# Performance work log

Measured on AMD Instinct MI355X. Metric: run time of the kernel, lower is better.

The kernel has to match this reference:

```python
import math
import jax, jax.numpy as jnp
import numpy as np

B, N, C = 2, 21760, 256
L, Hh, P = 4, 8, 4
Dh = C // Hh


def setup_inputs() -> dict:
    key = jax.random.key(0)
    ks = jax.random.split(key, 8)
    shapes = np.array([[128, 128], [64, 64], [32, 32], [16, 16]], dtype=np.int64)
    areas = shapes[:, 0] * shapes[:, 1]
    start_ids = np.concatenate([[0], np.cumsum(areas)[:-1]]).astype(np.int64)
    S = int(areas.sum())  # 21760

    in_feats = jax.random.normal(ks[0], (B, N, C), jnp.float32)
    sample_priors = jax.random.uniform(ks[1], (B, N, L, 2), jnp.float32)
    sample_feats = jax.random.normal(ks[2], (B, S, C), jnp.float32)

    # sampling_offsets: zero-init weight in torch; use small random so offsets vary,
    # bias is the canonical deformable-DETR grid init.
    W_off = jax.random.normal(ks[3], (C, Hh * L * P * 2), jnp.float32) * 0.01
    thetas = jnp.arange(Hh, dtype=jnp.float32) * (2.0 * math.pi / Hh)
    grid = jnp.stack([jnp.cos(thetas), jnp.sin(thetas)], axis=1)  # [Hh,2]
    grid = grid / jnp.max(jnp.abs(grid), axis=1, keepdims=True)
    grid = jnp.tile(grid[:, None, None, :], (1, L, P, 1))  # [Hh,L,P,2]
    sizes = jnp.arange(1, P + 1, dtype=jnp.float32).reshape(1, 1, P, 1)
    b_off = (sizes * grid).reshape(-1)  # [Hh*L*P*2]

    W_attn = jax.random.normal(ks[4], (C, Hh * L * P), jnp.float32) * 0.01
    b_attn = jnp.zeros((Hh * L * P,), jnp.float32)
    W_val = jax.random.normal(ks[5], (C, C), jnp.float32) / math.sqrt(C)
    b_val = jnp.zeros((C,), jnp.float32)
    W_out = jax.random.normal(ks[6], (C, C), jnp.float32) / math.sqrt(C)
    b_out = jnp.zeros((C,), jnp.float32)

    return dict(in_feats=in_feats, sample_priors=sample_priors, sample_feats=sample_feats,
                sample_map_shapes=jnp.asarray(shapes), sample_map_start_ids=jnp.asarray(start_ids),
                W_off=W_off, b_off=b_off, W_attn=W_attn, b_attn=b_attn,
                W_val=W_val, b_val=b_val, W_out=W_out, b_out=b_out)


def _msda_core(value, shapes_np, starts_np, loc, attn_w):
    """value: [B,S,Hh,Dh]; loc: [B,N,Hh,L,P,2] in [0,1]; attn_w: [B,N,Hh,L,P].
    Bilinear sampling matching grid_sample(align_corners=False, padding='zeros')."""
    b, n = loc.shape[:2]
    acc = jnp.zeros((b, n, Hh, Dh), value.dtype)
    for l in range(L):
        H_l, W_l = int(shapes_np[l, 0]), int(shapes_np[l, 1])
        s0 = int(starts_np[l])
        v = value[:, s0:s0 + H_l * W_l]  # [B,S_l,Hh,Dh]
        lx = loc[:, :, :, l, :, 0] * W_l - 0.5  # [B,N,Hh,P] pixel coords
        ly = loc[:, :, :, l, :, 1] * H_l - 0.5
        x0f, y0f = jnp.floor(lx), jnp.floor(ly)
        wx1, wy1 = lx - x0f, ly - y0f
        wx0, wy0 = 1.0 - wx1, 1.0 - wy1
        x0, y0 = x0f.astype(jnp.int32), y0f.astype(jnp.int32)

        def gather(xi, yi):
            valid = ((xi >= 0) & (xi < W_l) & (yi >= 0) & (yi < H_l)).astype(v.dtype)
            idx = jnp.clip(yi, 0, H_l - 1) * W_l + jnp.clip(xi, 0, W_l - 1)  # [B,N,Hh,P]
            idx_t = idx.transpose(0, 1, 3, 2).reshape(b, n * P, Hh)
            g = jnp.take_along_axis(v, idx_t[..., None], axis=1)  # [B,N*P,Hh,Dh]
            g = g.reshape(b, n, P, Hh, Dh).transpose(0, 1, 3, 2, 4)  # [B,N,Hh,P,Dh]
            return g * valid[..., None]

        samp = (gather(x0, y0) * (wx0 * wy0)[..., None]
                + gather(x0 + 1, y0) * (wx1 * wy0)[..., None]
                + gather(x0, y0 + 1) * (wx0 * wy1)[..., None]
                + gather(x0 + 1, y0 + 1) * (wx1 * wy1)[..., None])
        acc = acc + jnp.einsum('bnhpd,bnhp->bnhd', samp, attn_w[:, :, :, l, :])
    return acc


def reference(in_feats, sample_priors, sample_feats, sample_map_shapes, sample_map_start_ids,
              W_off, b_off, W_attn, b_attn, W_val, b_val, W_out, b_out):
    b, n = in_feats.shape[:2]
    # structural constants (level geometry)
    shapes_np = np.asarray(jax.device_get(sample_map_shapes))
    starts_np = np.asarray(jax.device_get(sample_map_start_ids))

    off = (in_feats @ W_off + b_off).reshape(b, n, Hh, L, P, 2)
    normalizer = jnp.flip(sample_map_shapes, axis=-1).astype(in_feats.dtype)  # [L,2] (W,H)
    loc = sample_priors[:, :, None, :, None, :] + off / normalizer[None, None, None, :, None, :]

    aw = jax.nn.softmax((in_feats @ W_attn + b_attn).reshape(b, n, Hh, L * P), axis=-1)
    aw = aw.reshape(b, n, Hh, L, P)

    value = (sample_feats @ W_val + b_val).reshape(b, -1, Hh, Dh)
    weighted = _msda_core(value, shapes_np, starts_np, loc, aw)  # [B,N,Hh,Dh]
    out = weighted.reshape(b, n, Hh * Dh) @ W_out + b_out
    return out
```

## Files before the change

kernel.cpp:

```cpp
#include <hip/hip_runtime.h>
#include <cstdint>

constexpr int kB = 2;
constexpr int kN = 21760;
constexpr int kC = 256;
constexpr int kH = 8;
constexpr int kS = 21760;
constexpr int kM = kB * kN;

typedef __attribute__((ext_vector_type(8))) short bf16x8;
typedef __attribute__((ext_vector_type(4))) float f32x4;
typedef __attribute__((ext_vector_type(8))) unsigned short us8;

__device__ __forceinline__ float bf2f(unsigned short u) {
  return __uint_as_float(((unsigned int)u) << 16);
}
__device__ __forceinline__ unsigned short f2bf(float f) {
  unsigned int u = __float_as_uint(f);
  u += 0x7fffu + ((u >> 16) & 1u);
  return (unsigned short)(u >> 16);
}
__device__ __forceinline__ void gld_lds16(const unsigned short* g, unsigned short* l) {
  __builtin_amdgcn_global_load_lds(
      (const __attribute__((address_space(1))) unsigned int*)g,
      (__attribute__((address_space(3))) unsigned int*)l, 16, 0, 0);
}

__global__ __launch_bounds__(256) void convert_act(
    const float* __restrict__ a, const float* __restrict__ b,
    unsigned short* __restrict__ da, unsigned short* __restrict__ db)
{
  const int tid = blockIdx.x * 256 + threadIdx.x;
  const int half = kM * 32;
  const float* src; unsigned short* dst; int id;
  if (tid < half) { src = a; dst = da; id = tid; }
  else            { src = b; dst = db; id = tid - half; }
  const int m = id >> 5;
  const int kb = (id & 31) * 8;
  const float4 x0 = *(const float4*)&src[(size_t)m * 256 + kb];
  const float4 x1 = *(const float4*)&src[(size_t)m * 256 + kb + 4];
  us8 o;
  o[0] = f2bf(x0.x); o[1] = f2bf(x0.y); o[2] = f2bf(x0.z); o[3] = f2bf(x0.w);
  o[4] = f2bf(x1.x); o[5] = f2bf(x1.y); o[6] = f2bf(x1.z); o[7] = f2bf(x1.w);
  *(us8*)&dst[(size_t)m * 256 + (kb ^ ((m & 7) << 3))] = o;
}

__global__ __launch_bounds__(256) void prep_weights(
    const float* __restrict__ Woff, const float* __restrict__ Wattn,
    const float* __restrict__ Wval, const float* __restrict__ Wout,
    unsigned short* __restrict__ BtOff, unsigned short* __restrict__ BtAttn,
    unsigned short* __restrict__ BtVal, unsigned short* __restrict__ BtOut)
{
  const int tid = blockIdx.x * 256 + threadIdx.x;
  const int r = tid >> 5;
  const int kb = (tid & 31) * 8;
  const float* W; unsigned short* Bt; int n, Nn;
  if (r < 256)      { W = Woff;  Bt = BtOff;  n = r;       Nn = 256; }
  else if (r < 384) { W = Wattn; Bt = BtAttn; n = r - 256; Nn = 128; }
  else if (r < 640) { W = Wval;  Bt = BtVal;  n = r - 384; Nn = 256; }
  else              { W = Wout;  Bt = BtOut;  n = r - 640; Nn = 256; }
  us8 o;
#pragma unroll
  for (int i = 0; i < 8; ++i) o[i] = f2bf(W[(size_t)(kb + i) * Nn + n]);
  *(us8*)&Bt[(size_t)n * 256 + (kb ^ ((n & 7) << 3))] = o;
}

template <int OMODE>
__global__ __launch_bounds__(256) void gemm_bf16(
    const unsigned short* __restrict__ A,
    const unsigned short* __restrict__ Bt,
    const float* __restrict__ bias,
    void* __restrict__ Cout, int Nn)
{
  __shared__ unsigned short As[128 * 64];
  __shared__ unsigned short Bs[128 * 64];
  const int t = threadIdx.x;
  const int w = t >> 6, l = t & 63;
  const int m0 = blockIdx.x * 128, n0 = blockIdx.y * 128;
  const int wm = w >> 1, wn = w & 1;

  f32x4 acc[4][4] = {};

  const int srow = l >> 3;
  const int skb  = (l & 7) * 8;

  for (int kt = 0; kt < 256; kt += 64) {
#pragma unroll
    for (int i = 0; i < 4; ++i) {
      const int c = i * 4 + w;
      const int row = c * 8 + srow;
      gld_lds16(A + (size_t)(m0 + row) * 256 + kt + skb, &As[c * 512]);
    }
#pragma unroll
    for (int i = 0; i < 4; ++i) {
      const int c = i * 4 + w;
      const int row = c * 8 + srow;
      gld_lds16(Bt + (size_t)(n0 + row) * 256 + kt + skb, &Bs[c * 512]);
    }
    __syncthreads();

#pragma unroll
    for (int s = 0; s < 2; ++s) {
      bf16x8 af[4], bfr[4];
      const int kf = s * 32 + ((l >> 4) * 8);
#pragma unroll
      for (int i = 0; i < 4; ++i) {
        const int row = wm * 64 + i * 16 + (l & 15);
        af[i] = *(const bf16x8*)&As[row * 64 + (kf ^ ((row & 7) << 3))];
      }
#pragma unroll
      for (int j = 0; j < 4; ++j) {
        const int col = wn * 64 + j * 16 + (l & 15);
        bfr[j] = *(const bf16x8*)&Bs[col * 64 + (kf ^ ((col & 7) << 3))];
      }
#pragma unroll
      for (int i = 0; i < 4; ++i)
#pragma unroll
        for (int j = 0; j < 4; ++j)
          acc[i][j] = __builtin_amdgcn_mfma_f32_16x16x32_bf16(af[i], bfr[j], acc[i][j], 0, 0, 0);
    }
    __syncthreads();
  }

  const int lr = l >> 4;
#pragma unroll
  for (int j = 0; j < 4; ++j) {
    const int col = n0 + wn * 64 + j * 16 + (l & 15);
    const float bv = bias[col];
#pragma unroll
    for (int i = 0; i < 4; ++i) {
      const int rbase = m0 + wm * 64 + i * 16 + lr * 4;
#pragma unroll
      for (int r = 0; r < 4; ++r) {
        const float v = acc[i][j][r] + bv;
        if (OMODE == 0) {
          ((float*)Cout)[(size_t)(rbase + r) * Nn + col] = v;
        } else if (OMODE == 1) {
          ((unsigned short*)Cout)[(size_t)(rbase + r) * Nn + col] = f2bf(v);
        } else {
          const int row = rbase + r;
          const int bb = row >= kS;
          const int s2 = row - bb * kS;
          ((unsigned short*)Cout)[((size_t)(bb * 8 + (col >> 5)) * kS + s2) * 32 + (col & 31)] = f2bf(v);
        }
      }
    }
  }
}

__global__ __launch_bounds__(256) void msda_kernel(
    const unsigned short* __restrict__ off_bf,
    const unsigned short* __restrict__ attn_bf,
    const unsigned short* __restrict__ val_bf,
    const float* __restrict__ priors,
    unsigned short* __restrict__ wgt)
{
  __shared__ int   s_mi[256 * 4];
  __shared__ float s_mw[256 * 4];
  const int q0 = blockIdx.x * 2;
  const int t = threadIdx.x;
  const int qh = t >> 4;
  const int q = q0 + (qh >> 3);
  const int h = qh & 7;

  {
    const int j = t & 15;
    const int lv = j >> 2;

    const float lgt = bf2f(attn_bf[(size_t)q * 128 + h * 16 + j]);
    float mx = lgt;
#pragma unroll
    for (int m = 8; m; m >>= 1) mx = fmaxf(mx, __shfl_xor(mx, m, 16));
    const float p = __expf(lgt - mx);
    float sum = p;
#pragma unroll
    for (int m = 8; m; m >>= 1) sum += __shfl_xor(sum, m, 16);
    const float wN = p / sum;

    const unsigned int oo = *(const unsigned int*)&off_bf[(size_t)q * 256 + (h * 16 + j) * 2];
    const float ox = bf2f((unsigned short)(oo & 0xffff));
    const float oy = bf2f((unsigned short)(oo >> 16));
    const float2 pr = *(const float2*)&priors[(size_t)q * 8 + lv * 2];

    const int Wl = 128 >> lv;
    const float fW = (float)Wl;
    const float lx = fmaf(pr.x, fW, ox) - 0.5f;
    const float ly = fmaf(pr.y, fW, oy) - 0.5f;
    const float x0f = floorf(lx), y0f = floorf(ly);
    const float wx1 = lx - x0f, wy1 = ly - y0f;
    const float wx0 = 1.f - wx1, wy0 = 1.f - wy1;
    const int x0 = (int)x0f, y0 = (int)y0f;
    const int start = (int)((0x5400500040000000ull >> (16 * lv)) & 0xffff);

    const bool vx0 = (x0 >= 0) & (x0 < Wl);
    const bool vx1 = (x0 + 1 >= 0) & (x0 + 1 < Wl);
    const bool vy0 = (y0 >= 0) & (y0 < Wl);
    const bool vy1 = (y0 + 1 >= 0) & (y0 + 1 < Wl);
    const int xc0 = min(max(x0, 0), Wl - 1);
    const int xc1 = min(max(x0 + 1, 0), Wl - 1);
    const int yc0 = min(max(y0, 0), Wl - 1);
    const int yc1 = min(max(y0 + 1, 0), Wl - 1);

    const int off_top = (start + yc0 * Wl + xc0) * 64;
    const int off_bot = (start + yc1 * Wl + xc0) * 64;
    const int dx = (xc1 - xc0) * 64;

    const int slot = j * 16 + (qh ^ (j & 3));
    int4 mi; mi.x = off_top; mi.y = off_bot; mi.z = dx; mi.w = 0;
    *(int4*)&s_mi[slot * 4] = mi;
    float4 mw;
    mw.x = (vx0 & vy0) ? wN * wx0 * wy0 : 0.f;
    mw.y = (vx0 & vy1) ? wN * wx0 * wy1 : 0.f;
    mw.z = (vx1 & vy0) ? wN * wx1 * wy0 : 0.f;
    mw.w = (vx1 & vy1) ? wN * wx1 * wy1 : 0.f;
    *(float4*)&s_mw[slot * 4] = mw;
  }
  __syncthreads();

  const int idx = t & 15;
  const int xsel = idx >> 3;
  const int ch8 = idx & 7;
  const int b = (q >= kN) ? 1 : 0;
  const char* base = (const char*)val_bf + ((size_t)(b * 8 + h) * kS) * 64 + ch8 * 8;

  float a0 = 0.f, a1 = 0.f, a2 = 0.f, a3 = 0.f;
#pragma unroll
  for (int j = 0; j < 16; ++j) {
    const int slot = j * 16 + (qh ^ (j & 3));
    const int4 md = *(const int4*)&s_mi[slot * 4];
    const float2 wv = *(const float2*)&s_mw[slot * 4 + xsel * 2];
    const int dxs = xsel ? md.z : 0;
    const uint2 vt = *(const uint2*)(base + (md.x + dxs));
    const uint2 vb = *(const uint2*)(base + (md.y + dxs));
    a0 = fmaf(wv.x, __uint_as_float(vt.x << 16), a0);
    a1 = fmaf(wv.x, __uint_as_float(vt.x & 0xffff0000u), a1);
    a2 = fmaf(wv.x, __uint_as_float(vt.y << 16), a2);
    a3 = fmaf(wv.x, __uint_as_float(vt.y & 0xffff0000u), a3);
    a0 = fmaf(wv.y, __uint_as_float(vb.x << 16), a0);
    a1 = fmaf(wv.y, __uint_as_float(vb.x & 0xffff0000u), a1);
    a2 = fmaf(wv.y, __uint_as_float(vb.y << 16), a2);
    a3 = fmaf(wv.y, __uint_as_float(vb.y & 0xffff0000u), a3);
  }

  a0 += __shfl_xor(a0, 8, 16);
  a1 += __shfl_xor(a1, 8, 16);
  a2 += __shfl_xor(a2, 8, 16);
  a3 += __shfl_xor(a3, 8, 16);

  if (xsel == 0) {
    const int c0 = h * 32 + ch8 * 4;
    const int dst = (c0 ^ ((q & 7) << 3));
    uint2 o;
    o.x = (unsigned int)f2bf(a0) | ((unsigned int)f2bf(a1) << 16);
    o.y = (unsigned int)f2bf(a2) | ((unsigned int)f2bf(a3) << 16);
    *(uint2*)&wgt[(size_t)q * 256 + dst] = o;
  }
}

extern "C" void kernel_launch(void* const* d_in, const int* in_sizes, int n_in,
                              void* d_out, int out_size, void* d_ws, size_t ws_size,
                              hipStream_t stream) {
  const float* in_feats = (const float*)d_in[0];
  const float* priors   = (const float*)d_in[1];
  const float* sfeats   = (const float*)d_in[2];
  const float* W_off  = (const float*)d_in[5];
  const float* b_off  = (const float*)d_in[6];
  const float* W_attn = (const float*)d_in[7];
  const float* b_attn = (const float*)d_in[8];
  const float* W_val  = (const float*)d_in[9];
  const float* b_val  = (const float*)d_in[10];
  const float* W_out  = (const float*)d_in[11];
  const float* b_out  = (const float*)d_in[12];
  float* out = (float*)d_out;

  unsigned short* in_bf   = (unsigned short*)d_ws;
  unsigned short* s_bf    = in_bf   + (size_t)kM * 256;
  unsigned short* off_bf  = s_bf    + (size_t)kM * 256;
  unsigned short* attn_bf = off_bf  + (size_t)kM * 256;
  unsigned short* val_bf  = attn_bf + (size_t)kM * 128;
  unsigned short* wgt_bf  = val_bf  + (size_t)kM * 256;
  unsigned short* BtOff   = wgt_bf  + (size_t)kM * 256;
  unsigned short* BtAttn  = BtOff   + 256 * 256;
  unsigned short* BtVal   = BtAttn  + 128 * 256;
  unsigned short* BtOut   = BtVal   + 256 * 256;

  const dim3 blk(256);

  convert_act<<<dim3(kM * 32 * 2 / 256), blk, 0, stream>>>(in_feats, sfeats, in_bf, s_bf);
  prep_weights<<<dim3(896 * 32 / 256), blk, 0, stream>>>(
      W_off, W_attn, W_val, W_out, BtOff, BtAttn, BtVal, BtOut);

  gemm_bf16<1><<<dim3(kM / 128, 2), blk, 0, stream>>>(in_bf, BtOff, b_off, off_bf, 256);
  gemm_bf16<1><<<dim3(kM / 128, 1), blk, 0, stream>>>(in_bf, BtAttn, b_attn, attn_bf, 128);
  gemm_bf16<2><<<dim3(kM / 128, 2), blk, 0, stream>>>(s_bf, BtVal, b_val, val_bf, 256);

  msda_kernel<<<dim3(kM / 2), blk, 0, stream>>>(off_bf, attn_bf, val_bf, priors, wgt_bf);

  gemm_bf16<0><<<dim3(kM / 128, 2), blk, 0, stream>>>(wgt_bf, BtOut, b_out, out, 256);
}
```

Baseline: 180.1 us.

## Store offsets/attn head-major and remap MSDA blocks to one head plane per block

The offset and attention GEMMs now write head-major layouts, so each head's 16 logits and 32 offsets sit contiguously per query. The MSDA kernel gives each block 16 queries of a single (batch, head) plane, so the value gathers of neighbouring blocks hit the same plane for better cache locality. Each lane now gathers one corner with 16-byte loads across 8 channels, instead of two 8-byte loads, and partial sums are reduced with two xor-shuffles. The corner records are packed (offset, weight) pairs in padded shared memory. The risk is more shuffle work and the strided head-major writes in the GEMM epilogues.

```diff
diff --git a/kernel.cpp b/kernel.cpp
--- a/kernel.cpp
+++ b/kernel.cpp
@@ -20,6 +20,8 @@
   u += 0x7fffu + ((u >> 16) & 1u);
   return (unsigned short)(u >> 16);
 }
+__device__ __forceinline__ float blo(unsigned int v) { return __uint_as_float(v << 16); }
+__device__ __forceinline__ float bhi(unsigned int v) { return __uint_as_float(v & 0xffff0000u); }
 __device__ __forceinline__ void gld_lds16(const unsigned short* g, unsigned short* l) {
   __builtin_amdgcn_global_load_lds(
       (const __attribute__((address_space(1))) unsigned int*)g,
@@ -133,15 +135,19 @@
 #pragma unroll
       for (int r = 0; r < 4; ++r) {
         const float v = acc[i][j][r] + bv;
+        const int row = rbase + r;
         if (OMODE == 0) {
-          ((float*)Cout)[(size_t)(rbase + r) * Nn + col] = v;
+          ((float*)Cout)[(size_t)row * Nn + col] = v;
         } else if (OMODE == 1) {
-          ((unsigned short*)Cout)[(size_t)(rbase + r) * Nn + col] = f2bf(v);
-        } else {
-          const int row = rbase + r;
+          ((unsigned short*)Cout)[(size_t)row * Nn + col] = f2bf(v);
+        } else if (OMODE == 2) {
           const int bb = row >= kS;
           const int s2 = row - bb * kS;
           ((unsigned short*)Cout)[((size_t)(bb * 8 + (col >> 5)) * kS + s2) * 32 + (col & 31)] = f2bf(v);
+        } else if (OMODE == 3) {
+          ((unsigned short*)Cout)[((size_t)(col >> 4) * kM + row) * 16 + (col & 15)] = f2bf(v);
+        } else {
+          ((unsigned short*)Cout)[((size_t)(col >> 5) * kM + row) * 32 + (col & 31)] = f2bf(v);
         }
       }
     }
@@ -149,25 +155,26 @@
 }
 
 __global__ __launch_bounds__(256) void msda_kernel(
-    const unsigned short* __restrict__ off_bf,
-    const unsigned short* __restrict__ attn_bf,
+    const unsigned short* __restrict__ off_hm,
+    const unsigned short* __restrict__ attn_hm,
     const unsigned short* __restrict__ val_bf,
     const float* __restrict__ priors,
     unsigned short* __restrict__ wgt)
 {
-  __shared__ int   s_mi[256 * 4];
-  __shared__ float s_mw[256 * 4];
-  const int q0 = blockIdx.x * 2;
+  __shared__ int s_rec[16 * 136];
+  const int bid = blockIdx.x;
+  const int plane = bid & 15;
+  const int chunk = bid >> 4;
+  const int b = plane >> 3, h = plane & 7;
   const int t = threadIdx.x;
-  const int qh = t >> 4;
-  const int q = q0 + (qh >> 3);
-  const int h = qh & 7;
+  const int ql = t >> 4;
+  const int q = b * kN + chunk * 16 + ql;
 
   {
     const int j = t & 15;
     const int lv = j >> 2;
 
-    const float lgt = bf2f(attn_bf[(size_t)q * 128 + h * 16 + j]);
+    const float lgt = bf2f(attn_hm[((size_t)h * kM + q) * 16 + j]);
     float mx = lgt;
 #pragma unroll
     for (int m = 8; m; m >>= 1) mx = fmaxf(mx, __shfl_xor(mx, m, 16));
@@ -177,9 +184,9 @@
     for (int m = 8; m; m >>= 1) sum += __shfl_xor(sum, m, 16);
     const float wN = p / sum;
 
-    const unsigned int oo = *(const unsigned int*)&off_bf[(size_t)q * 256 + (h * 16 + j) * 2];
-    const float ox = bf2f((unsigned short)(oo & 0xffff));
-    const float oy = bf2f((unsigned short)(oo >> 16));
+    const unsigned int oo = *(const unsigned int*)&off_hm[((size_t)h * kM + q) * 32 + j * 2];
+    const float ox = blo(oo);
+    const float oy = bhi(oo);
     const float2 pr = *(const float2*)&priors[(size_t)q * 8 + lv * 2];
 
     const int Wl = 128 >> lv;
@@ -201,59 +208,57 @@
     const int yc0 = min(max(y0, 0), Wl - 1);
     const int yc1 = min(max(y0 + 1, 0), Wl - 1);
 
-    const int off_top = (start + yc0 * Wl + xc0) * 64;
-    const int off_bot = (start + yc1 * Wl + xc0) * 64;
-    const int dx = (xc1 - xc0) * 64;
-
-    const int slot = j * 16 + (qh ^ (j & 3));
-    int4 mi; mi.x = off_top; mi.y = off_bot; mi.z = dx; mi.w = 0;
-    *(int4*)&s_mi[slot * 4] = mi;
-    float4 mw;
-    mw.x = (vx0 & vy0) ? wN * wx0 * wy0 : 0.f;
-    mw.y = (vx0 & vy1) ? wN * wx0 * wy1 : 0.f;
-    mw.z = (vx1 & vy0) ? wN * wx1 * wy0 : 0.f;
-    mw.w = (vx1 & vy1) ? wN * wx1 * wy1 : 0.f;
-    *(float4*)&s_mw[slot * 4] = mw;
+    const int rt = start + yc0 * Wl;
+    const int rb = start + yc1 * Wl;
+
+    int4 r0, r1;
+    r0.x = (rt + xc0) * 64; r0.y = __float_as_int((vx0 & vy0) ? wN * wx0 * wy0 : 0.f);
+    r0.z = (rt + xc1) * 64; r0.w = __float_as_int((vx1 & vy0) ? wN * wx1 * wy0 : 0.f);
+    r1.x = (rb + xc0) * 64; r1.y = __float_as_int((vx0 & vy1) ? wN * wx0 * wy1 : 0.f);
+    r1.z = (rb + xc1) * 64; r1.w = __float_as_int((vx1 & vy1) ? wN * wx1 * wy1 : 0.f);
+
+    const int base = ql * 136 + j * 8;
+    *(int4*)&s_rec[base] = r0;
+    *(int4*)&s_rec[base + 4] = r1;
   }
   __syncthreads();
 
-  const int idx = t & 15;
-  const int xsel = idx >> 3;
-  const int ch8 = idx & 7;
-  const int b = (q >= kN) ? 1 : 0;
-  const char* base = (const char*)val_bf + ((size_t)(b * 8 + h) * kS) * 64 + ch8 * 8;
+  const int lane = t & 15;
+  const int c = lane >> 2;
+  const int k = lane & 3;
+  const char* plane_base = (const char*)val_bf + (size_t)plane * kS * 64 + k * 16;
+  const int* rp = &s_rec[ql * 136 + c * 2];
 
   float a0 = 0.f, a1 = 0.f, a2 = 0.f, a3 = 0.f;
+  float a4 = 0.f, a5 = 0.f, a6 = 0.f, a7 = 0.f;
 #pragma unroll
   for (int j = 0; j < 16; ++j) {
-    const int slot = j * 16 + (qh ^ (j & 3));
-    const int4 md = *(const int4*)&s_mi[slot * 4];
-    const float2 wv = *(const float2*)&s_mw[slot * 4 + xsel * 2];
-    const int dxs = xsel ? md.z : 0;
-    const uint2 vt = *(const uint2*)(base + (md.x + dxs));
-    const uint2 vb = *(const uint2*)(base + (md.y + dxs));
-    a0 = fmaf(wv.x, __uint_as_float(vt.x << 16), a0);
-    a1 = fmaf(wv.x, __uint_as_float(vt.x & 0xffff0000u), a1);
-    a2 = fmaf(wv.x, __uint_as_float(vt.y << 16), a2);
-    a3 = fmaf(wv.x, __uint_as_float(vt.y & 0xffff0000u), a3);
-    a0 = fmaf(wv.y, __uint_as_float(vb.x << 16), a0);
-    a1 = fmaf(wv.y, __uint_as_float(vb.x & 0xffff0000u), a1);
-    a2 = fmaf(wv.y, __uint_as_float(vb.y << 16), a2);
-    a3 = fmaf(wv.y, __uint_as_float(vb.y & 0xffff0000u), a3);
-  }
-
-  a0 += __shfl_xor(a0, 8, 16);
-  a1 += __shfl_xor(a1, 8, 16);
-  a2 += __shfl_xor(a2, 8, 16);
-  a3 += __shfl_xor(a3, 8, 16);
-
-  if (xsel == 0) {
-    const int c0 = h * 32 + ch8 * 4;
-    const int dst = (c0 ^ ((q & 7) << 3));
-    uint2 o;
+    const int2 r = *(const int2*)&rp[j * 8];
+    const float w = __int_as_float(r.y);
+    const uint4 v = *(const uint4*)(plane_base + r.x);
+    a0 = fmaf(w, blo(v.x), a0); a1 = fmaf(w, bhi(v.x), a1);
+    a2 = fmaf(w, blo(v.y), a2); a3 = fmaf(w, bhi(v.y), a3);
+    a4 = fmaf(w, blo(v.z), a4); a5 = fmaf(w, bhi(v.z), a5);
+    a6 = fmaf(w, blo(v.w), a6); a7 = fmaf(w, bhi(v.w), a7);
+  }
+
+#pragma unroll
+  for (int m = 4; m <= 8; m <<= 1) {
+    a0 += __shfl_xor(a0, m); a1 += __shfl_xor(a1, m);
+    a2 += __shfl_xor(a2, m); a3 += __shfl_xor(a3, m);
+    a4 += __shfl_xor(a4, m); a5 += __shfl_xor(a5, m);
+    a6 += __shfl_xor(a6, m); a7 += __shfl_xor(a7, m);
+  }
+
+  if (c == 0) {
+    const int c0 = h * 32 + k * 8;
+    const int dst = c0 ^ ((q & 7) << 3);
+    uint4 o;
     o.x = (unsigned int)f2bf(a0) | ((unsigned int)f2bf(a1) << 16);
     o.y = (unsigned int)f2bf(a2) | ((unsigned int)f2bf(a3) << 16);
-    *(uint2*)&wgt[(size_t)q * 256 + dst] = o;
+    o.z = (unsigned int)f2bf(a4) | ((unsigned int)f2bf(a5) << 16);
+    o.w = (unsigned int)f2bf(a6) | ((unsigned int)f2bf(a7) << 16);
+    *(uint4*)&wgt[(size_t)q * 256 + dst] = o;
   }
 }
 
@@ -290,8 +295,8 @@
   prep_weights<<<dim3(896 * 32 / 256), blk, 0, stream>>>(
       W_off, W_attn, W_val, W_out, BtOff, BtAttn, BtVal, BtOut);
 
-  gemm_bf16<1><<<dim3(kM / 128, 2), blk, 0, stream>>>(in_bf, BtOff, b_off, off_bf, 256);
-  gemm_bf16<1><<<dim3(kM / 128, 1), blk, 0, stream>>>(in_bf, BtAttn, b_attn, attn_bf, 128);
+  gemm_bf16<4><<<dim3(kM / 128, 2), blk, 0, stream>>>(in_bf, BtOff, b_off, off_bf, 256);
+  gemm_bf16<3><<<dim3(kM / 128, 1), blk, 0, stream>>>(in_bf, BtAttn, b_attn, attn_bf, 128);
   gemm_bf16<2><<<dim3(kM / 128, 2), blk, 0, stream>>>(s_bf, BtVal, b_val, val_bf, 256);
 
   msda_kernel<<<dim3(kM / 2), blk, 0, stream>>>(off_bf, attn_bf, val_bf, priors, wgt_bf);
```

Result: faster. 152.6 us (-15.3%).
